# Kernel tuning notes

Hardware: AMD Instinct MI355X
Metric: run time of the kernel (lower is better)

The kernel has to match this reference:

```python
import jax, jax.numpy as jnp
import numpy as np

B = 16            # number of graphs
IN_DIM, HID, OUT = 16, 64, 32
SIZES = np.array([256 + 16 * g for g in range(B)], dtype=np.int64)  # ragged graph sizes
N_TOT = int(SIZES.sum())            # 6016 nodes total
N_MAX = int(SIZES.max())            # 496
N_PAIRS = int((SIZES ** 2).sum())   # 2349056 valid (i,j) pairs


def setup_inputs() -> dict:
    key = jax.random.key(0)
    k_ape, k_w1, k_w2 = jax.random.split(key, 3)
    ape = jax.random.normal(k_ape, (N_TOT, IN_DIM), dtype=jnp.float32)
    W1 = jax.random.normal(k_w1, (IN_DIM, HID), dtype=jnp.float32) / np.sqrt(IN_DIM)
    b1 = jnp.zeros((HID,), dtype=jnp.float32)
    W2 = jax.random.normal(k_w2, (HID, OUT), dtype=jnp.float32) / np.sqrt(HID)
    b2 = jnp.zeros((OUT,), dtype=jnp.float32)
    batch = jnp.asarray(np.repeat(np.arange(B), SIZES), dtype=jnp.int32)
    return dict(ape=ape, W1=W1, b1=b1, W2=W2, b2=b2, batch=batch,
                num_graphs=B, n_max=N_MAX, n_pairs=N_PAIRS)


def reference(ape, W1, b1, W2, b2, batch, num_graphs, n_max, n_pairs):
    n_tot, in_dim = ape.shape
    # per-graph node counts and start offsets (equivalent of torch.bincount)
    counts = jax.ops.segment_sum(jnp.ones((n_tot,), jnp.int32), batch,
                                 num_segments=num_graphs)
    starts = jnp.cumsum(counts) - counts
    pos = jnp.arange(n_tot, dtype=jnp.int32) - starts[batch]
    # to_dense_batch: scatter ragged nodes into [B, n_max, in_dim] padded tensor
    dense = jnp.zeros((num_graphs, n_max, in_dim), ape.dtype).at[batch, pos].set(ape)
    # MLP: Linear -> ReLU -> Linear  (applied on padded dense batch as in the original)
    t = jax.nn.relu(dense @ W1 + b1) @ W2 + b2          # [B, n_max, OUT]
    # pairwise outer-sum: rpe[b,i,j] = t[b,i] + t[b,j]
    rpe = t[:, :, None, :] + t[:, None, :, :]           # [B, n_max, n_max, OUT]
    # from_dense_adj: gather valid (i<n_b, j<n_b) entries back to ragged layout
    node_mask = jnp.arange(n_max)[None, :] < counts[:, None]      # [B, n_max]
    pair_mask = node_mask[:, :, None] & node_mask[:, None, :]     # [B, n_max, n_max]
    bi, ii, jj = jnp.nonzero(pair_mask, size=n_pairs)             # static size -> jit-safe
    return rpe[bi, ii, jj]                                        # [n_pairs, OUT]
```

## Files before the change

kernel.cpp:

```cpp
#include <hip/hip_runtime.h>

#define IN_DIM   16
#define HID      64
#define OUT      32
#define NGRAPH   16
#define N_TOT    6016
#define N_PAIRS  2349056
#define TOTAL_F4 (N_PAIRS * (OUT / 4))

__host__ __device__ constexpr unsigned sumsq(unsigned n) {
    return n * (n + 1u) * (2u * n + 1u) / 6u;
}
__host__ __device__ constexpr unsigned poff_of(unsigned g) {
    return 256u * (sumsq(g + 15u) - 1240u);
}
static_assert(poff_of(3)  == 222464u,  "poff check");
static_assert(poff_of(15) == 2103040u, "poff check");
static_assert(poff_of(15) + 496u * 496u == (unsigned)N_PAIRS, "total check");

__global__ __launch_bounds__(256) void mlp_kernel(
    const float* __restrict__ ape, const float* __restrict__ W1,
    const float* __restrict__ b1,  const float* __restrict__ W2,
    const float* __restrict__ b2,  float* __restrict__ T)
{
    __shared__ float Hs[8][HID];
    __shared__ float W2s[HID * OUT];

    for (int idx = threadIdx.x; idx < HID * OUT; idx += 256)
        W2s[idx] = W2[idx];

    const int nl   = threadIdx.x >> 5;
    const int c    = threadIdx.x & 31;
    const int node = blockIdx.x * 8 + nl;

    float acc0 = b1[c];
    float acc1 = b1[c + 32];
    const float* a = ape + node * IN_DIM;
#pragma unroll
    for (int d = 0; d < IN_DIM; ++d) {
        const float av = a[d];
        acc0 += av * W1[d * HID + c];
        acc1 += av * W1[d * HID + c + 32];
    }
    Hs[nl][c]      = fmaxf(acc0, 0.0f);
    Hs[nl][c + 32] = fmaxf(acc1, 0.0f);
    __syncthreads();

    float t = b2[c];
#pragma unroll
    for (int k = 0; k < HID; ++k)
        t += Hs[nl][k] * W2s[k * OUT + c];
    T[node * OUT + c] = t;
}

__global__ __launch_bounds__(256) void pair_kernel(
    const float4* __restrict__ T4, float4* __restrict__ out4)
{
    const unsigned q = blockIdx.x * 256u + threadIdx.x;
    if (q >= (unsigned)TOTAL_F4) return;

    const unsigned p  = q >> 3;
    const unsigned c4 = q & 7;

    unsigned g = 0;
#pragma unroll
    for (unsigned k = 1; k < NGRAPH; ++k)
        g += (p >= poff_of(k)) ? 1u : 0u;

    const unsigned poffg = poff_of(g);
    const unsigned n     = 256u + (g << 4);
    const unsigned start = (g * (g + 31u)) << 3;

    const unsigned lp = p - poffg;
    const unsigned i  = (lp >> 4) / (g + 16u);
    const unsigned j  = lp - i * n;

    const float4 va = T4[(start + i) * (OUT / 4) + c4];
    const float4 vb = T4[(start + j) * (OUT / 4) + c4];
    out4[q] = make_float4(va.x + vb.x, va.y + vb.y, va.z + vb.z, va.w + vb.w);
}

extern "C" void kernel_launch(void* const* d_in, const int* in_sizes, int n_in,
                              void* d_out, int out_size, void* d_ws, size_t ws_size,
                              hipStream_t stream) {
    const float* ape = (const float*)d_in[0];
    const float* W1  = (const float*)d_in[1];
    const float* b1  = (const float*)d_in[2];
    const float* W2  = (const float*)d_in[3];
    const float* b2  = (const float*)d_in[4];

    float* T = (float*)d_ws;

    mlp_kernel<<<N_TOT / 8, 256, 0, stream>>>(ape, W1, b1, W2, b2, T);
    pair_kernel<<<TOTAL_F4 / 256, 256, 0, stream>>>((const float4*)T,
                                                    (float4*)d_out);
}
```

Measured before the change: 306.0 us.

## Assign one block per output row and use nontemporal stores in pair kernel

The pair kernel now launches one block per global node row instead of one thread per output float4. Each block finds its graph from the row index, loads t_i once, and loops over j in strides of 32 rows. Output writes use nontemporal stores. This drops the per-element graph search and integer division and reuses the row vector. The cost is a small grid (6016 blocks) with loops of uneven length, and nontemporal stores change how the output interacts with the cache.

Result: slower. 318.2 us (+4.0%).

```diff
diff --git a/kernel.cpp b/kernel.cpp
--- a/kernel.cpp
+++ b/kernel.cpp
@@ -8,15 +8,21 @@
 #define N_PAIRS  2349056
 #define TOTAL_F4 (N_PAIRS * (OUT / 4))
 
+typedef float f32x4 __attribute__((ext_vector_type(4)));
+
 __host__ __device__ constexpr unsigned sumsq(unsigned n) {
     return n * (n + 1u) * (2u * n + 1u) / 6u;
 }
 __host__ __device__ constexpr unsigned poff_of(unsigned g) {
     return 256u * (sumsq(g + 15u) - 1240u);
 }
+__host__ __device__ constexpr unsigned start_of(unsigned g) {
+    return (g * (g + 31u)) << 3;
+}
 static_assert(poff_of(3)  == 222464u,  "poff check");
 static_assert(poff_of(15) == 2103040u, "poff check");
 static_assert(poff_of(15) + 496u * 496u == (unsigned)N_PAIRS, "total check");
+static_assert(start_of(16) == (unsigned)N_TOT, "row total check");
 
 __global__ __launch_bounds__(256) void mlp_kernel(
     const float* __restrict__ ape, const float* __restrict__ W1,
@@ -54,30 +60,34 @@
 }
 
 __global__ __launch_bounds__(256) void pair_kernel(
-    const float4* __restrict__ T4, float4* __restrict__ out4)
+    const f32x4* __restrict__ T4, f32x4* __restrict__ out4)
 {
-    const unsigned q = blockIdx.x * 256u + threadIdx.x;
-    if (q >= (unsigned)TOTAL_F4) return;
-
-    const unsigned p  = q >> 3;
-    const unsigned c4 = q & 7;
+    const unsigned r = blockIdx.x;
 
     unsigned g = 0;
 #pragma unroll
     for (unsigned k = 1; k < NGRAPH; ++k)
-        g += (p >= poff_of(k)) ? 1u : 0u;
+        g += (r >= start_of(k)) ? 1u : 0u;
 
+    const unsigned start = start_of(g);
+    const unsigned n     = 256u + (g << 4);
+    const unsigned i     = r - start;
     const unsigned poffg = poff_of(g);
-    const unsigned n     = 256u + (g << 4);
-    const unsigned start = (g * (g + 31u)) << 3;
 
-    const unsigned lp = p - poffg;
-    const unsigned i  = (lp >> 4) / (g + 16u);
-    const unsigned j  = lp - i * n;
+    const unsigned c4 = threadIdx.x & 7u;
+    const unsigned jl = threadIdx.x >> 3;
 
-    const float4 va = T4[(start + i) * (OUT / 4) + c4];
-    const float4 vb = T4[(start + j) * (OUT / 4) + c4];
-    out4[q] = make_float4(va.x + vb.x, va.y + vb.y, va.z + vb.z, va.w + vb.w);
+    const f32x4 ti = T4[r * 8u + c4];
+
+    const unsigned obase = (poffg + i * n) * 8u;
+
+    const f32x4* __restrict__ pj = T4   + (start + jl) * 8u + c4;
+    f32x4*       __restrict__ po = out4 + obase + jl * 8u + c4;
+
+    for (unsigned j = jl; j < n; j += 32u, pj += 256u, po += 256u) {
+        const f32x4 tj = *pj;
+        __builtin_nontemporal_store(ti + tj, po);
+    }
 }
 
 extern "C" void kernel_launch(void* const* d_in, const int* in_sizes, int n_in,
@@ -92,6 +102,5 @@
     float* T = (float*)d_ws;
 
     mlp_kernel<<<N_TOT / 8, 256, 0, stream>>>(ape, W1, b1, W2, b2, T);
-    pair_kernel<<<TOTAL_F4 / 256, 256, 0, stream>>>((const float4*)T,
-                                                    (float4*)d_out);
+    pair_kernel<<<N_TOT, 256, 0, stream>>>((const f32x4*)T, (f32x4*)d_out);
 }
```
